# Performance work log

Hardware: AMD Instinct MI355X
Metric: run time of the kernel (lower is better)

Reference implementation:

```python
import jax, jax.numpy as jnp
import numpy as np
from jax import lax

B, T, I, H, C = 64, 512, 512, 1024, 1000


def _lstm_layer(x, W_ih, W_hh, b_ih, b_hh):
    # x: [B, T, in]; W_ih: [4H, in]; W_hh: [4H, H]; biases: [4H]
    # Precompute input projections for all timesteps (one big GEMM).
    xW = jnp.einsum('bti,gi->btg', x, W_ih) + b_ih + b_hh  # [B, T, 4H]
    h0 = jnp.zeros((x.shape[0], W_hh.shape[1]), x.dtype)
    c0 = jnp.zeros_like(h0)

    def step(carry, xw_t):
        h, c = carry
        gates = xw_t + h @ W_hh.T  # [B, 4H]
        i, f, g, o = jnp.split(gates, 4, axis=-1)  # PyTorch gate order i,f,g,o
        i = jax.nn.sigmoid(i)
        f = jax.nn.sigmoid(f)
        g = jnp.tanh(g)
        o = jax.nn.sigmoid(o)
        c = f * c + i * g
        h = o * jnp.tanh(c)
        return (h, c), h

    (h_T, c_T), hs = lax.scan(step, (h0, c0), jnp.swapaxes(xW, 0, 1))
    return jnp.swapaxes(hs, 0, 1), h_T  # [B, T, H], [B, H]


def setup_inputs() -> dict:
    key = jax.random.key(0)
    ks = jax.random.split(key, 11)
    s_i = 1.0 / np.sqrt(H)
    u = lambda k, shape: jax.random.uniform(k, shape, jnp.float32, -s_i, s_i)
    return {
        'x': jax.random.normal(ks[0], (B, T, I), jnp.float32),
        'W_ih0': u(ks[1], (4 * H, I)),
        'W_hh0': u(ks[2], (4 * H, H)),
        'b_ih0': u(ks[3], (4 * H,)),
        'b_hh0': u(ks[4], (4 * H,)),
        'W_ih1': u(ks[5], (4 * H, H)),
        'W_hh1': u(ks[6], (4 * H, H)),
        'b_ih1': u(ks[7], (4 * H,)),
        'b_hh1': u(ks[8], (4 * H,)),
        'W_d': u(ks[9], (C, H)),
        'b_d': u(ks[10], (C,)),
    }


def reference(x, W_ih0, W_hh0, b_ih0, b_hh0, W_ih1, W_hh1, b_ih1, b_hh1, W_d, b_d):
    h1_seq, _ = _lstm_layer(x, W_ih0, W_hh0, b_ih0, b_hh0)
    _, h_last = _lstm_layer(h1_seq, W_ih1, W_hh1, b_ih1, b_hh1)
    return h_last @ W_d.T + b_d  # [B, num_classes]
```

## Files before the change

### kernel.cpp

```cpp
#include <hip/hip_runtime.h>

typedef short short8 __attribute__((ext_vector_type(8)));
typedef float f32x4 __attribute__((ext_vector_type(4)));
typedef float f32x16 __attribute__((ext_vector_type(16)));
typedef int i32x4 __attribute__((ext_vector_type(4)));
typedef unsigned short u16;
typedef unsigned long long u64;

#define NBLK 256
#define BDIM 512
#define BB 64
#define TT 512
#define II 512
#define HH 1024
#define NCLS 1000
#define HBUF (BB*HH)

__device__ __forceinline__ u16 f2bf(float f) {
  union { float f; unsigned u; } v; v.f = f;
  unsigned u = v.u;
  u += 0x7fffu + ((u >> 16) & 1u);
  return (u16)(u >> 16);
}

__device__ __forceinline__ short8 cvt8(f32x4 a, f32x4 b) {
  short8 v;
  v[0] = (short)f2bf(a[0]); v[1] = (short)f2bf(a[1]);
  v[2] = (short)f2bf(a[2]); v[3] = (short)f2bf(a[3]);
  v[4] = (short)f2bf(b[0]); v[5] = (short)f2bf(b[1]);
  v[6] = (short)f2bf(b[2]); v[7] = (short)f2bf(b[3]);
  return v;
}

__device__ __forceinline__ unsigned ld_rlx(const unsigned* p) {
  return __hip_atomic_load(p, __ATOMIC_RELAXED, __HIP_MEMORY_SCOPE_AGENT);
}
__device__ __forceinline__ void st_rlx(unsigned* p, unsigned v) {
  __hip_atomic_store(p, v, __ATOMIC_RELAXED, __HIP_MEMORY_SCOPE_AGENT);
}
__device__ __forceinline__ void wave_wait_ge(const unsigned* p, unsigned tgt) {
  while (ld_rlx(p) < tgt) __builtin_amdgcn_s_sleep(1);
}

__global__ void cvt_x(const float* __restrict__ x, u16* __restrict__ xb, int n8) {
  int i = blockIdx.x * blockDim.x + threadIdx.x;
  const int stride = gridDim.x * blockDim.x;
  for (; i < n8; i += stride) {
    f32x4 a = ((const f32x4*)x)[2 * i];
    f32x4 b = ((const f32x4*)x)[2 * i + 1];
    ((short8*)xb)[i] = cvt8(a, b);
  }
}

#define ISSUE8(arr, OFF)                                                     \
  _Pragma("unroll") for (int i_ = 0; i_ < 8; ++i_)                           \
    asm volatile("global_load_dwordx4 %0, %1, off sc0 sc1"                   \
                 : "=v"(arr[i_]) : "v"(lanep + ((OFF) + i_) * 16));
#define MFMA8(arr, OFF)                                                      \
  _Pragma("unroll") for (int i_ = 0; i_ < 8; ++i_) {                         \
    union { i32x4 q; short8 s; } u_; u_.q = arr[i_];                         \
    acc = __builtin_amdgcn_mfma_f32_32x32x16_bf16(u_.s, breg[B0 + (OFF) + i_],\
                                                  acc, 0, 0, 0); }
#define VMWAIT0 asm volatile("s_waitcnt vmcnt(0)" ::: "memory")
#define VMWAIT8 asm volatile("s_waitcnt vmcnt(8)" ::: "memory")
#define SCHEDB  __builtin_amdgcn_sched_barrier(0)

template<int N, int B0, int MH>
__device__ __forceinline__ void run_coh(const u16* lanep,
                                        const short8 (&breg)[MH], f32x16& acc) {
  static_assert(N == 8 || N == 16 || N == 24 || N == 32, "");
  i32x4 avA[8], avB[8];
  if constexpr (N == 8) {
    ISSUE8(avA, 0);
    VMWAIT0; SCHEDB; MFMA8(avA, 0);
  } else if constexpr (N == 16) {
    ISSUE8(avA, 0); ISSUE8(avB, 8);
    VMWAIT8; SCHEDB; MFMA8(avA, 0);
    VMWAIT0; SCHEDB; MFMA8(avB, 8);
  } else if constexpr (N == 24) {
    ISSUE8(avA, 0); ISSUE8(avB, 8);
    VMWAIT8; SCHEDB; MFMA8(avA, 0); ISSUE8(avA, 16);
    VMWAIT8; SCHEDB; MFMA8(avB, 8);
    VMWAIT0; SCHEDB; MFMA8(avA, 16);
  } else {
    ISSUE8(avA, 0); ISSUE8(avB, 8);
    VMWAIT8; SCHEDB; MFMA8(avA, 0); ISSUE8(avA, 16);
    VMWAIT8; SCHEDB; MFMA8(avB, 8); ISSUE8(avB, 24);
    VMWAIT8; SCHEDB; MFMA8(avA, 16);
    VMWAIT0; SCHEDB; MFMA8(avB, 24);
  }
}

template<int N, int B0, int MH>
__device__ __forceinline__ void run_pb(const u16* lanep,
                                       const short8 (&breg)[MH], f32x16& acc) {
#pragma unroll
  for (int i = 0; i < N; ++i) {
    short8 av = *(const short8*)(lanep + i * 16);
    acc = __builtin_amdgcn_mfma_f32_32x32x16_bf16(av, breg[B0 + i], acc, 0, 0, 0);
  }
}

template<int N, int B0, int MH>
__device__ __forceinline__ void run_pf(const float* lanep,
                                       const short8 (&breg)[MH], f32x16& acc) {
#pragma unroll
  for (int i = 0; i < N; ++i) {
    short8 av = cvt8(*(const f32x4*)(lanep + i * 16),
                     *(const f32x4*)(lanep + i * 16 + 4));
    acc = __builtin_amdgcn_mfma_f32_32x32x16_bf16(av, breg[B0 + i], acc, 0, 0, 0);
  }
}

template<bool XBF>
__global__ __launch_bounds__(BDIM, 2) void lstm2_fused(
    const float* __restrict__ x, const u16* __restrict__ xb,
    const float* __restrict__ Wih0, const float* __restrict__ Whh0,
    const float* __restrict__ bih0, const float* __restrict__ bhh0,
    const float* __restrict__ Wih1, const float* __restrict__ Whh1,
    const float* __restrict__ bih1, const float* __restrict__ bhh1,
    u16* __restrict__ ring,
    u16* __restrict__ h1buf,
    float* __restrict__ h1f,
    unsigned* __restrict__ bar)
{
  __shared__ u16 wlds[32 * 2048];
  __shared__ float blds[32];
  float (*g4)[64][32] = (float(*)[64][32])((char*)wlds + 98304);

  const bool isL1 = (blockIdx.x >= 128);
  const int wgl = isL1 ? (int)blockIdx.x - 128 : (int)blockIdx.x;
  const int j0 = wgl * 8;
  const int KX = isL1 ? HH : II;
  const int RL = KX + HH;
  const int ROWB = RL * 2;
  const float* Wih = isL1 ? Wih1 : Wih0;
  const float* Whh = isL1 ? Whh1 : Whh0;

  {
    const int cpr = RL / 8;
    for (int idx = threadIdx.x; idx < 32 * cpr; idx += BDIM) {
      int n = idx / cpr, cb = idx - n * cpr;
      int r = ((n >> 3) << 10) + j0 + (n & 7);
      int k = cb * 8;
      const float* src = (k < KX) ? (Wih + (size_t)r * KX + k)
                                  : (Whh + (size_t)r * HH + (k - KX));
      f32x4 a = *(const f32x4*)src;
      f32x4 b = *(const f32x4*)(src + 4);
      short8 v = cvt8(a, b);
      unsigned byte = (unsigned)(n * ROWB + k * 2) ^ ((unsigned)(n & 7) << 4);
      *(short8*)((char*)wlds + byte) = v;
    }
    if (threadIdx.x < 32) {
      int n = threadIdx.x;
      int r = ((n >> 3) << 10) + j0 + (n & 7);
      blds[n] = (isL1 ? bih1[r] : bih0[r]) + (isL1 ? bhh1[r] : bhh0[r]);
    }
  }
  __syncthreads();

  const int lane = threadIdx.x & 63;
  const int wid = threadIdx.x >> 6;
  const int mp = wid & 1, kq = wid >> 1;
  const int row_a = mp * 32 + (lane & 31);
  const int sub8 = (lane >> 5) << 3;
  const char* wch = (const char*)wlds;

  const int tb = threadIdx.x >> 3, tj = threadIdx.x & 7;

  unsigned* const arrA = bar;
  unsigned* const relA = bar + 64;
  unsigned* const arrB = bar + 256;
  unsigned* const relB = bar + 320;

  float c_state = 0.f;

  auto step_tail = [&](const f32x16& acc, u16* hout, unsigned ringtgt, bool wf,
                       unsigned* arr, unsigned* rel, int t) {
    const int col = lane & 31;
    const int rbase = mp * 32 + ((lane >> 5) << 2);
#pragma unroll
    for (int r = 0; r < 16; ++r) {
      int brow = rbase + (r & 3) + ((r >> 2) << 3);
      g4[kq][brow][col] = acc[r];
    }
    __syncthreads();
    float gv[4];
#pragma unroll
    for (int g = 0; g < 4; ++g)
      gv[g] = g4[0][tb][g * 8 + tj] + g4[1][tb][g * 8 + tj]
            + g4[2][tb][g * 8 + tj] + g4[3][tb][g * 8 + tj] + blds[g * 8 + tj];
    float gi = 1.f / (1.f + __expf(-gv[0]));
    float gf = 1.f / (1.f + __expf(-gv[1]));
    float e2 = __expf(2.f * fminf(15.f, fmaxf(-15.f, gv[2])));
    float gg = (e2 - 1.f) / (e2 + 1.f);
    float go = 1.f / (1.f + __expf(-gv[3]));
    c_state = gf * c_state + gi * gg;
    float e2c = __expf(2.f * fminf(15.f, fmaxf(-15.f, c_state)));
    float th = (e2c - 1.f) / (e2c + 1.f);
    float hval = go * th;
    if (ringtgt) wave_wait_ge(relB, ringtgt);
    unsigned hu = (unsigned)f2bf(hval);
    unsigned nbv = (unsigned)__shfl_xor((int)hu, 1);
    if ((tj & 1) == 0) {
      unsigned packed = hu | (nbv << 16);
      unsigned* dst = (unsigned*)(hout + (size_t)tb * HH + j0 + tj);
      st_rlx(dst, packed);
    }
    if (wf) h1f[(size_t)tb * HH + j0 + tj] = hval;
    __syncthreads();
    if (threadIdx.x == 0) {
      unsigned old = atomicAdd(arr, 1u);
      if (old == (unsigned)(128 * (t + 1) - 1)) st_rlx(rel, (unsigned)(t + 1));
    }
  };

  if (!isL1) {
    short8 breg[24];
#pragma unroll
    for (int i = 0; i < 24; ++i) {
      int k = (kq * 24 + i) * 16 + sub8;
      unsigned byte = ((unsigned)((lane & 31) * ROWB + k * 2))
                      ^ ((unsigned)(lane & 7) << 4);
      breg[i] = *(const short8*)(wch + byte);
    }
    __syncthreads();

    for (int t = 0; t < TT; ++t) {
      f32x16 acc = {};
      const u16* hb = ring + (size_t)((t + 2) % 3) * HBUF + (size_t)row_a * HH;
      if (XBF) {
        const u16* xl = xb + (size_t)t * II + (size_t)row_a * ((size_t)TT * II)
                        + kq * 384 + sub8;
        if (kq == 0)      run_pb<24, 0>(xl, breg, acc);
        else if (kq == 1) { run_pb<8, 0>(xl, breg, acc);
                            wave_wait_ge(relA, (unsigned)t);
                            run_coh<16, 8>(hb + 0 + sub8, breg, acc); }
        else if (kq == 2) { wave_wait_ge(relA, (unsigned)t);
                            run_coh<24, 0>(hb + 256 + sub8, breg, acc); }
        else              { wave_wait_ge(relA, (unsigned)t);
                            run_coh<24, 0>(hb + 640 + sub8, breg, acc); }
      } else {
        const float* xl = x + (size_t)t * II + (size_t)row_a * ((size_t)TT * II)
                          + kq * 384 + sub8;
        if (kq == 0)      run_pf<24, 0>(xl, breg, acc);
        else if (kq == 1) { run_pf<8, 0>(xl, breg, acc);
                            wave_wait_ge(relA, (unsigned)t);
                            run_coh<16, 8>(hb + 0 + sub8, breg, acc); }
        else if (kq == 2) { wave_wait_ge(relA, (unsigned)t);
                            run_coh<24, 0>(hb + 256 + sub8, breg, acc); }
        else              { wave_wait_ge(relA, (unsigned)t);
                            run_coh<24, 0>(hb + 640 + sub8, breg, acc); }
      }
      step_tail(acc, ring + (size_t)(t % 3) * HBUF,
                (t >= 3) ? (unsigned)(t - 2) : 0u, false, arrA, relA, t);
    }
  } else {
    short8 breg[32];
#pragma unroll
    for (int i = 0; i < 32; ++i) {
      int k = (kq * 32 + i) * 16 + sub8;
      unsigned byte = ((unsigned)((lane & 31) * ROWB + k * 2))
                      ^ ((unsigned)(lane & 7) << 4);
      breg[i] = *(const short8*)(wch + byte);
    }
    __syncthreads();

    for (int t = 0; t < TT; ++t) {
      f32x16 acc = {};
      if (kq < 2) {
        wave_wait_ge(relA, (unsigned)(t + 1));
        const u16* lp = ring + (size_t)(t % 3) * HBUF + (size_t)row_a * HH
                        + kq * 512 + sub8;
        run_coh<32, 0>(lp, breg, acc);
      } else {
        wave_wait_ge(relB, (unsigned)t);
        const u16* lp = h1buf + (size_t)((t + 1) & 1) * HBUF
                        + (size_t)row_a * HH + (kq - 2) * 512 + sub8;
        run_coh<32, 0>(lp, breg, acc);
      }
      step_tail(acc, h1buf + (size_t)(t & 1) * HBUF, 0u, t == TT - 1,
                arrB, relB, t);
    }
  }
}

__global__ void dense_out(const float* __restrict__ h1, const float* __restrict__ Wd,
                          const float* __restrict__ bd, float* __restrict__ out)
{
  const int b  = threadIdx.x & 63;
  const int cl = threadIdx.x >> 6;
  const int cc = blockIdx.x * 4 + cl;
  float acc = 0.f;
  const float* hrow = h1 + (size_t)b * HH;
  const float* wrow = Wd + (size_t)cc * HH;
#pragma unroll 8
  for (int k = 0; k < HH; k += 4) {
    f32x4 hv = *(const f32x4*)(hrow + k);
    f32x4 wv = *(const f32x4*)(wrow + k);
    acc += hv[0] * wv[0] + hv[1] * wv[1] + hv[2] * wv[2] + hv[3] * wv[3];
  }
  out[(size_t)b * NCLS + cc] = acc + bd[cc];
}

extern "C" void kernel_launch(void* const* d_in, const int* in_sizes, int n_in,
                              void* d_out, int out_size, void* d_ws, size_t ws_size,
                              hipStream_t stream)
{
  (void)in_sizes; (void)n_in; (void)out_size;
  const float* x    = (const float*)d_in[0];
  const float* Wih0 = (const float*)d_in[1];
  const float* Whh0 = (const float*)d_in[2];
  const float* bih0 = (const float*)d_in[3];
  const float* bhh0 = (const float*)d_in[4];
  const float* Wih1 = (const float*)d_in[5];
  const float* Whh1 = (const float*)d_in[6];
  const float* bih1 = (const float*)d_in[7];
  const float* bhh1 = (const float*)d_in[8];
  const float* Wd   = (const float*)d_in[9];
  const float* bd   = (const float*)d_in[10];

  unsigned* bar = (unsigned*)d_ws;
  float* h1f  = (float*)((char*)d_ws + 4096);
  u16* h1buf  = (u16*)((char*)d_ws + 272 * 1024);
  u16* ring   = (u16*)((char*)d_ws + 528 * 1024);
  u16* xb     = (u16*)((char*)d_ws + (1u << 20));

  const size_t needA = (1u << 20) + (size_t)BB * TT * II * 2;
  const bool tierA = (ws_size >= needA);

  hipMemsetAsync(d_ws, 0, 912 * 1024, stream);

  if (tierA) {
    hipLaunchKernelGGL(cvt_x, dim3(2048), dim3(256), 0, stream,
                       x, xb, (int)((size_t)BB * TT * II / 8));
    hipLaunchKernelGGL((lstm2_fused<true>), dim3(NBLK), dim3(BDIM), 0, stream,
                       x, xb, Wih0, Whh0, bih0, bhh0, Wih1, Whh1, bih1, bhh1,
                       ring, h1buf, h1f, bar);
  } else {
    hipLaunchKernelGGL((lstm2_fused<false>), dim3(NBLK), dim3(BDIM), 0, stream,
                       x, xb, Wih0, Whh0, bih0, bhh0, Wih1, Whh1, bih1, bhh1,
                       ring, h1buf, h1f, bar);
  }
  hipLaunchKernelGGL(dense_out, dim3(250), dim3(256), 0, stream, h1f, Wd, bd,
                     (float*)d_out);
}
```

Before: 4.866 ms.

## Split grid-wide step barrier into eight group counters polled in parallel

The single global arrival counter per layer, which all 128 blocks hit with one atomicAdd each step, is replaced by eight counters with 16 blocks each, spaced 128 bytes apart. Waiters now poll all eight release flags at once, one per lane, and proceed only when every group has reached the target. The aim is to cut atomic contention and serialization on one cache line in the per-timestep barrier. In exchange, each poll issues eight loads per wave, and the host must zero the larger barrier region.

```diff
diff --git a/kernel.cpp b/kernel.cpp
--- a/kernel.cpp
+++ b/kernel.cpp
@@ -38,8 +38,14 @@
 __device__ __forceinline__ void st_rlx(unsigned* p, unsigned v) {
   __hip_atomic_store(p, v, __ATOMIC_RELAXED, __HIP_MEMORY_SCOPE_AGENT);
 }
-__device__ __forceinline__ void wave_wait_ge(const unsigned* p, unsigned tgt) {
-  while (ld_rlx(p) < tgt) __builtin_amdgcn_s_sleep(1);
+__device__ __forceinline__ void wave_wait_all8(const unsigned* base, unsigned tgt,
+                                               int lane) {
+  const unsigned* p = base + (unsigned)(lane & 7) * 32;
+  for (;;) {
+    unsigned v = ld_rlx(p);
+    if (__all((int)(v >= tgt))) break;
+    __builtin_amdgcn_s_sleep(1);
+  }
 }
 
 __global__ void cvt_x(const float* __restrict__ x, u16* __restrict__ xb, int n8) {
@@ -131,6 +137,7 @@
   const bool isL1 = (blockIdx.x >= 128);
   const int wgl = isL1 ? (int)blockIdx.x - 128 : (int)blockIdx.x;
   const int j0 = wgl * 8;
+  const int grp = wgl >> 4;
   const int KX = isL1 ? HH : II;
   const int RL = KX + HH;
   const int ROWB = RL * 2;
@@ -169,9 +176,9 @@
   const int tb = threadIdx.x >> 3, tj = threadIdx.x & 7;
 
   unsigned* const arrA = bar;
-  unsigned* const relA = bar + 64;
-  unsigned* const arrB = bar + 256;
-  unsigned* const relB = bar + 320;
+  unsigned* const relA = bar + 256;
+  unsigned* const arrB = bar + 512;
+  unsigned* const relB = bar + 768;
 
   float c_state = 0.f;
 
@@ -199,7 +206,7 @@
     float e2c = __expf(2.f * fminf(15.f, fmaxf(-15.f, c_state)));
     float th = (e2c - 1.f) / (e2c + 1.f);
     float hval = go * th;
-    if (ringtgt) wave_wait_ge(relB, ringtgt);
+    if (ringtgt) wave_wait_all8(relB, ringtgt, lane);
     unsigned hu = (unsigned)f2bf(hval);
     unsigned nbv = (unsigned)__shfl_xor((int)hu, 1);
     if ((tj & 1) == 0) {
@@ -210,8 +217,9 @@
     if (wf) h1f[(size_t)tb * HH + j0 + tj] = hval;
     __syncthreads();
     if (threadIdx.x == 0) {
-      unsigned old = atomicAdd(arr, 1u);
-      if (old == (unsigned)(128 * (t + 1) - 1)) st_rlx(rel, (unsigned)(t + 1));
+      unsigned old = atomicAdd(arr + grp * 32, 1u);
+      if (old == (unsigned)(16 * (t + 1) - 1))
+        st_rlx(rel + grp * 32, (unsigned)(t + 1));
     }
   };
 
@@ -234,22 +242,22 @@
                         + kq * 384 + sub8;
         if (kq == 0)      run_pb<24, 0>(xl, breg, acc);
         else if (kq == 1) { run_pb<8, 0>(xl, breg, acc);
-                            wave_wait_ge(relA, (unsigned)t);
+                            wave_wait_all8(relA, (unsigned)t, lane);
                             run_coh<16, 8>(hb + 0 + sub8, breg, acc); }
-        else if (kq == 2) { wave_wait_ge(relA, (unsigned)t);
+        else if (kq == 2) { wave_wait_all8(relA, (unsigned)t, lane);
                             run_coh<24, 0>(hb + 256 + sub8, breg, acc); }
-        else              { wave_wait_ge(relA, (unsigned)t);
+        else              { wave_wait_all8(relA, (unsigned)t, lane);
                             run_coh<24, 0>(hb + 640 + sub8, breg, acc); }
       } else {
         const float* xl = x + (size_t)t * II + (size_t)row_a * ((size_t)TT * II)
                           + kq * 384 + sub8;
         if (kq == 0)      run_pf<24, 0>(xl, breg, acc);
         else if (kq == 1) { run_pf<8, 0>(xl, breg, acc);
-                            wave_wait_ge(relA, (unsigned)t);
+                            wave_wait_all8(relA, (unsigned)t, lane);
                             run_coh<16, 8>(hb + 0 + sub8, breg, acc); }
-        else if (kq == 2) { wave_wait_ge(relA, (unsigned)t);
+        else if (kq == 2) { wave_wait_all8(relA, (unsigned)t, lane);
                             run_coh<24, 0>(hb + 256 + sub8, breg, acc); }
-        else              { wave_wait_ge(relA, (unsigned)t);
+        else              { wave_wait_all8(relA, (unsigned)t, lane);
                             run_coh<24, 0>(hb + 640 + sub8, breg, acc); }
       }
       step_tail(acc, ring + (size_t)(t % 3) * HBUF,
@@ -269,12 +277,12 @@
     for (int t = 0; t < TT; ++t) {
       f32x16 acc = {};
       if (kq < 2) {
-        wave_wait_ge(relA, (unsigned)(t + 1));
+        wave_wait_all8(relA, (unsigned)(t + 1), lane);
         const u16* lp = ring + (size_t)(t % 3) * HBUF + (size_t)row_a * HH
                         + kq * 512 + sub8;
         run_coh<32, 0>(lp, breg, acc);
       } else {
-        wave_wait_ge(relB, (unsigned)t);
+        wave_wait_all8(relB, (unsigned)t, lane);
         const u16* lp = h1buf + (size_t)((t + 1) & 1) * HBUF
                         + (size_t)row_a * HH + (kq - 2) * 512 + sub8;
         run_coh<32, 0>(lp, breg, acc);
```

Measured after the change: 5.280 ms. 8.5% more time.

## Halve persistent blocks with 16 hidden units each and dual accumulators per wave

Applied to the files above, without the earlier changes.

The fused two-layer LSTM kernel now runs 128 persistent blocks (64 per layer) instead of 256, each owning 16 hidden units. Each wave now handles 32 gate rows across all 64 batch rows, using two MFMA accumulators that share the same register-resident weight fragments. Weights are loaded straight from global memory into registers, with the LDS staging copy removed. The aim is to cut the number of blocks taking part in each per-step grid barrier and to reuse each weight register twice. The cost is twice the activation loads and twice the gate math per block on the serial critical path.

```diff
diff --git a/kernel.cpp b/kernel.cpp
--- a/kernel.cpp
+++ b/kernel.cpp
@@ -5,9 +5,8 @@
 typedef float f32x16 __attribute__((ext_vector_type(16)));
 typedef int i32x4 __attribute__((ext_vector_type(4)));
 typedef unsigned short u16;
-typedef unsigned long long u64;
-
-#define NBLK 256
+
+#define NBLK 128
 #define BDIM 512
 #define BB 64
 #define TT 512
@@ -52,63 +51,72 @@
   }
 }
 
-#define ISSUE8(arr, OFF)                                                     \
-  _Pragma("unroll") for (int i_ = 0; i_ < 8; ++i_)                           \
+#define ISSUE42(buf, OFF)                                                    \
+  _Pragma("unroll") for (int i_ = 0; i_ < 4; ++i_) {                         \
     asm volatile("global_load_dwordx4 %0, %1, off sc0 sc1"                   \
-                 : "=v"(arr[i_]) : "v"(lanep + ((OFF) + i_) * 16));
-#define MFMA8(arr, OFF)                                                      \
-  _Pragma("unroll") for (int i_ = 0; i_ < 8; ++i_) {                         \
-    union { i32x4 q; short8 s; } u_; u_.q = arr[i_];                         \
-    acc = __builtin_amdgcn_mfma_f32_32x32x16_bf16(u_.s, breg[B0 + (OFF) + i_],\
-                                                  acc, 0, 0, 0); }
+                 : "=v"(buf[2 * i_])     : "v"(lp0 + ((OFF) + i_) * 16));    \
+    asm volatile("global_load_dwordx4 %0, %1, off sc0 sc1"                   \
+                 : "=v"(buf[2 * i_ + 1]) : "v"(lp1 + ((OFF) + i_) * 16)); }
+#define MFMA42(buf, OFF)                                                     \
+  _Pragma("unroll") for (int i_ = 0; i_ < 4; ++i_) {                         \
+    union { i32x4 q; short8 s; } uA_, uB_;                                   \
+    uA_.q = buf[2 * i_]; uB_.q = buf[2 * i_ + 1];                            \
+    acc0 = __builtin_amdgcn_mfma_f32_32x32x16_bf16(uA_.s,                    \
+             breg[B0 + (OFF) + i_], acc0, 0, 0, 0);                          \
+    acc1 = __builtin_amdgcn_mfma_f32_32x32x16_bf16(uB_.s,                    \
+             breg[B0 + (OFF) + i_], acc1, 0, 0, 0); }
 #define VMWAIT0 asm volatile("s_waitcnt vmcnt(0)" ::: "memory")
 #define VMWAIT8 asm volatile("s_waitcnt vmcnt(8)" ::: "memory")
 #define SCHEDB  __builtin_amdgcn_sched_barrier(0)
 
 template<int N, int B0, int MH>
-__device__ __forceinline__ void run_coh(const u16* lanep,
-                                        const short8 (&breg)[MH], f32x16& acc) {
-  static_assert(N == 8 || N == 16 || N == 24 || N == 32, "");
-  i32x4 avA[8], avB[8];
-  if constexpr (N == 8) {
-    ISSUE8(avA, 0);
-    VMWAIT0; SCHEDB; MFMA8(avA, 0);
-  } else if constexpr (N == 16) {
-    ISSUE8(avA, 0); ISSUE8(avB, 8);
-    VMWAIT8; SCHEDB; MFMA8(avA, 0);
-    VMWAIT0; SCHEDB; MFMA8(avB, 8);
-  } else if constexpr (N == 24) {
-    ISSUE8(avA, 0); ISSUE8(avB, 8);
-    VMWAIT8; SCHEDB; MFMA8(avA, 0); ISSUE8(avA, 16);
-    VMWAIT8; SCHEDB; MFMA8(avB, 8);
-    VMWAIT0; SCHEDB; MFMA8(avA, 16);
-  } else {
-    ISSUE8(avA, 0); ISSUE8(avB, 8);
-    VMWAIT8; SCHEDB; MFMA8(avA, 0); ISSUE8(avA, 16);
-    VMWAIT8; SCHEDB; MFMA8(avB, 8); ISSUE8(avB, 24);
-    VMWAIT8; SCHEDB; MFMA8(avA, 16);
-    VMWAIT0; SCHEDB; MFMA8(avB, 24);
+__device__ __forceinline__ void run_coh2(const u16* lp0, const u16* lp1,
+                                         const short8 (&breg)[MH],
+                                         f32x16& acc0, f32x16& acc1) {
+  static_assert(N % 4 == 0 && N >= 8, "");
+  constexpr int C = N / 4;
+  i32x4 bufA[8], bufB[8];
+  ISSUE42(bufA, 0);
+  ISSUE42(bufB, 4);
+#pragma unroll
+  for (int c = 0; c < C; ++c) {
+    if (c + 2 < C) {
+      VMWAIT8; SCHEDB;
+      if (c & 1) { MFMA42(bufB, c * 4); ISSUE42(bufB, (c + 2) * 4); }
+      else       { MFMA42(bufA, c * 4); ISSUE42(bufA, (c + 2) * 4); }
+    } else if (c + 1 < C) {
+      VMWAIT8; SCHEDB;
+      if (c & 1) { MFMA42(bufB, c * 4); } else { MFMA42(bufA, c * 4); }
+    } else {
+      VMWAIT0; SCHEDB;
+      if (c & 1) { MFMA42(bufB, c * 4); } else { MFMA42(bufA, c * 4); }
+    }
   }
 }
 
 template<int N, int B0, int MH>
-__device__ __forceinline__ void run_pb(const u16* lanep,
-                                       const short8 (&breg)[MH], f32x16& acc) {
+__device__ __forceinline__ void run_px2(const u16* lp0, const u16* lp1,
+                                        const short8 (&breg)[MH],
+                                        f32x16& acc0, f32x16& acc1) {
 #pragma unroll
   for (int i = 0; i < N; ++i) {
-    short8 av = *(const short8*)(lanep + i * 16);
-    acc = __builtin_amdgcn_mfma_f32_32x32x16_bf16(av, breg[B0 + i], acc, 0, 0, 0);
+    short8 a0 = *(const short8*)(lp0 + i * 16);
+    short8 a1 = *(const short8*)(lp1 + i * 16);
+    acc0 = __builtin_amdgcn_mfma_f32_32x32x16_bf16(a0, breg[B0 + i], acc0, 0, 0, 0);
+    acc1 = __builtin_amdgcn_mfma_f32_32x32x16_bf16(a1, breg[B0 + i], acc1, 0, 0, 0);
   }
 }
 
 template<int N, int B0, int MH>
-__device__ __forceinline__ void run_pf(const float* lanep,
-                                       const short8 (&breg)[MH], f32x16& acc) {
+__device__ __forceinline__ void run_pf2(const float* lp0, const float* lp1,
+                                        const short8 (&breg)[MH],
+                                        f32x16& acc0, f32x16& acc1) {
 #pragma unroll
   for (int i = 0; i < N; ++i) {
-    short8 av = cvt8(*(const f32x4*)(lanep + i * 16),
-                     *(const f32x4*)(lanep + i * 16 + 4));
-    acc = __builtin_amdgcn_mfma_f32_32x32x16_bf16(av, breg[B0 + i], acc, 0, 0, 0);
+    short8 a0 = cvt8(*(const f32x4*)(lp0 + i * 16), *(const f32x4*)(lp0 + i * 16 + 4));
+    short8 a1 = cvt8(*(const f32x4*)(lp1 + i * 16), *(const f32x4*)(lp1 + i * 16 + 4));
+    acc0 = __builtin_amdgcn_mfma_f32_32x32x16_bf16(a0, breg[B0 + i], acc0, 0, 0, 0);
+    acc1 = __builtin_amdgcn_mfma_f32_32x32x16_bf16(a1, breg[B0 + i], acc1, 0, 0, 0);
   }
 }
 
@@ -124,94 +132,88 @@
     float* __restrict__ h1f,
     unsigned* __restrict__ bar)
 {
-  __shared__ u16 wlds[32 * 2048];
-  __shared__ float blds[32];
-  float (*g4)[64][32] = (float(*)[64][32])((char*)wlds + 98304);
-
-  const bool isL1 = (blockIdx.x >= 128);
-  const int wgl = isL1 ? (int)blockIdx.x - 128 : (int)blockIdx.x;
-  const int j0 = wgl * 8;
-  const int KX = isL1 ? HH : II;
-  const int RL = KX + HH;
-  const int ROWB = RL * 2;
-  const float* Wih = isL1 ? Wih1 : Wih0;
-  const float* Whh = isL1 ? Whh1 : Whh0;
-
-  {
-    const int cpr = RL / 8;
-    for (int idx = threadIdx.x; idx < 32 * cpr; idx += BDIM) {
-      int n = idx / cpr, cb = idx - n * cpr;
-      int r = ((n >> 3) << 10) + j0 + (n & 7);
-      int k = cb * 8;
-      const float* src = (k < KX) ? (Wih + (size_t)r * KX + k)
-                                  : (Whh + (size_t)r * HH + (k - KX));
-      f32x4 a = *(const f32x4*)src;
-      f32x4 b = *(const f32x4*)(src + 4);
-      short8 v = cvt8(a, b);
-      unsigned byte = (unsigned)(n * ROWB + k * 2) ^ ((unsigned)(n & 7) << 4);
-      *(short8*)((char*)wlds + byte) = v;
-    }
-    if (threadIdx.x < 32) {
-      int n = threadIdx.x;
-      int r = ((n >> 3) << 10) + j0 + (n & 7);
-      blds[n] = (isL1 ? bih1[r] : bih0[r]) + (isL1 ? bhh1[r] : bhh0[r]);
-    }
-  }
-  __syncthreads();
+  __shared__ float g4[4][64][65];
+  __shared__ float blds[64];
+
+  const bool isL1 = (blockIdx.x >= 64);
+  const int wgl = isL1 ? (int)blockIdx.x - 64 : (int)blockIdx.x;
+  const int j0 = wgl * 16;
 
   const int lane = threadIdx.x & 63;
   const int wid = threadIdx.x >> 6;
-  const int mp = wid & 1, kq = wid >> 1;
-  const int row_a = mp * 32 + (lane & 31);
+  const int gr = wid & 1, kq = wid >> 1;
   const int sub8 = (lane >> 5) << 3;
-  const char* wch = (const char*)wlds;
-
-  const int tb = threadIdx.x >> 3, tj = threadIdx.x & 7;
+  const int rl = gr * 32 + (lane & 31);
+  const int rglob = ((rl >> 4) << 10) + j0 + (rl & 15);
+
+  if (threadIdx.x < 64) {
+    int u = threadIdx.x;
+    int r = ((u >> 4) << 10) + j0 + (u & 15);
+    blds[u] = isL1 ? (bih1[r] + bhh1[r]) : (bih0[r] + bhh0[r]);
+  }
+  __syncthreads();
+
+  const int tb = threadIdx.x >> 3;
+  const int uu = (threadIdx.x & 7) << 1;
 
   unsigned* const arrA = bar;
   unsigned* const relA = bar + 64;
-  unsigned* const arrB = bar + 256;
-  unsigned* const relB = bar + 320;
-
-  float c_state = 0.f;
-
-  auto step_tail = [&](const f32x16& acc, u16* hout, unsigned ringtgt, bool wf,
-                       unsigned* arr, unsigned* rel, int t) {
-    const int col = lane & 31;
-    const int rbase = mp * 32 + ((lane >> 5) << 2);
+  unsigned* const arrB = bar + 128;
+  unsigned* const relB = bar + 192;
+
+  float cst0 = 0.f, cst1 = 0.f;
+
+  auto step_tail = [&](const f32x16& acc0, const f32x16& acc1, u16* hout,
+                       unsigned ringtgt, bool wf, unsigned* arr, unsigned* rel,
+                       int t) {
 #pragma unroll
     for (int r = 0; r < 16; ++r) {
-      int brow = rbase + (r & 3) + ((r >> 2) << 3);
-      g4[kq][brow][col] = acc[r];
+      int brow = (r & 3) + ((r >> 2) << 3) + ((lane >> 5) << 2);
+      g4[kq][brow][rl] = acc0[r];
+      g4[kq][brow + 32][rl] = acc1[r];
     }
     __syncthreads();
-    float gv[4];
-#pragma unroll
-    for (int g = 0; g < 4; ++g)
-      gv[g] = g4[0][tb][g * 8 + tj] + g4[1][tb][g * 8 + tj]
-            + g4[2][tb][g * 8 + tj] + g4[3][tb][g * 8 + tj] + blds[g * 8 + tj];
-    float gi = 1.f / (1.f + __expf(-gv[0]));
-    float gf = 1.f / (1.f + __expf(-gv[1]));
-    float e2 = __expf(2.f * fminf(15.f, fmaxf(-15.f, gv[2])));
-    float gg = (e2 - 1.f) / (e2 + 1.f);
-    float go = 1.f / (1.f + __expf(-gv[3]));
-    c_state = gf * c_state + gi * gg;
-    float e2c = __expf(2.f * fminf(15.f, fmaxf(-15.f, c_state)));
-    float th = (e2c - 1.f) / (e2c + 1.f);
-    float hval = go * th;
+    float hva, hvb;
+    {
+      float gi = g4[0][tb][uu] + g4[1][tb][uu] + g4[2][tb][uu] + g4[3][tb][uu] + blds[uu];
+      float gf = g4[0][tb][16+uu] + g4[1][tb][16+uu] + g4[2][tb][16+uu] + g4[3][tb][16+uu] + blds[16+uu];
+      float gg = g4[0][tb][32+uu] + g4[1][tb][32+uu] + g4[2][tb][32+uu] + g4[3][tb][32+uu] + blds[32+uu];
+      float go = g4[0][tb][48+uu] + g4[1][tb][48+uu] + g4[2][tb][48+uu] + g4[3][tb][48+uu] + blds[48+uu];
+      gi = 1.f / (1.f + __expf(-gi));
+      gf = 1.f / (1.f + __expf(-gf));
+      go = 1.f / (1.f + __expf(-go));
+      float e2 = __expf(2.f * fminf(15.f, fmaxf(-15.f, gg)));
+      gg = (e2 - 1.f) / (e2 + 1.f);
+      cst0 = gf * cst0 + gi * gg;
+      float e2c = __expf(2.f * fminf(15.f, fmaxf(-15.f, cst0)));
+      hva = go * (e2c - 1.f) / (e2c + 1.f);
+    }
+    {
+      int u1 = uu + 1;
+      float gi = g4[0][tb][u1] + g4[1][tb][u1] + g4[2][tb][u1] + g4[3][tb][u1] + blds[u1];
+      float gf = g4[0][tb][16+u1] + g4[1][tb][16+u1] + g4[2][tb][16+u1] + g4[3][tb][16+u1] + blds[16+u1];
+      float gg = g4[0][tb][32+u1] + g4[1][tb][32+u1] + g4[2][tb][32+u1] + g4[3][tb][32+u1] + blds[32+u1];
+      float go = g4[0][tb][48+u1] + g4[1][tb][48+u1] + g4[2][tb][48+u1] + g4[3][tb][48+u1] + blds[48+u1];
+      gi = 1.f / (1.f + __expf(-gi));
+      gf = 1.f / (1.f + __expf(-gf));
+      go = 1.f / (1.f + __expf(-go));
+      float e2 = __expf(2.f * fminf(15.f, fmaxf(-15.f, gg)));
+      gg = (e2 - 1.f) / (e2 + 1.f);
+      cst1 = gf * cst1 + gi * gg;
+      float e2c = __expf(2.f * fminf(15.f, fmaxf(-15.f, cst1)));
+      hvb = go * (e2c - 1.f) / (e2c + 1.f);
+    }
     if (ringtgt) wave_wait_ge(relB, ringtgt);
-    unsigned hu = (unsigned)f2bf(hval);
-    unsigned nbv = (unsigned)__shfl_xor((int)hu, 1);
-    if ((tj & 1) == 0) {
-      unsigned packed = hu | (nbv << 16);
-      unsigned* dst = (unsigned*)(hout + (size_t)tb * HH + j0 + tj);
-      st_rlx(dst, packed);
-    }
-    if (wf) h1f[(size_t)tb * HH + j0 + tj] = hval;
+    unsigned packed = (unsigned)f2bf(hva) | ((unsigned)f2bf(hvb) << 16);
+    st_rlx((unsigned*)(hout + (size_t)tb * HH + j0 + uu), packed);
+    if (wf) {
+      h1f[(size_t)tb * HH + j0 + uu] = hva;
+      h1f[(size_t)tb * HH + j0 + uu + 1] = hvb;
+    }
     __syncthreads();
     if (threadIdx.x == 0) {
       unsigned old = atomicAdd(arr, 1u);
-      if (old == (unsigned)(128 * (t + 1) - 1)) st_rlx(rel, (unsigned)(t + 1));
+      if (old == (unsigned)(64 * (t + 1) - 1)) st_rlx(rel, (unsigned)(t + 1));
     }
   };
 
@@ -219,67 +221,71 @@
     short8 breg[24];
 #pragma unroll
     for (int i = 0; i < 24; ++i) {
-      int k = (kq * 24 + i) * 16 + sub8;
-      unsigned byte = ((unsigned)((lane & 31) * ROWB + k * 2))
-                      ^ ((unsigned)(lane & 7) << 4);
-      breg[i] = *(const short8*)(wch + byte);
-    }
-    __syncthreads();
+      int k = kq * 384 + i * 16 + sub8;
+      const float* src = (k < II) ? (Wih0 + (size_t)rglob * II + k)
+                                  : (Whh0 + (size_t)rglob * HH + (k - II));
+      breg[i] = cvt8(*(const f32x4*)src, *(const f32x4*)(src + 4));
+    }
 
     for (int t = 0; t < TT; ++t) {
-      f32x16 acc = {};
-      const u16* hb = ring + (size_t)((t + 2) % 3) * HBUF + (size_t)row_a * HH;
+      f32x16 acc0 = {}, acc1 = {};
+      const u16* hb = ring + (size_t)((t + 2) % 3) * HBUF
+                      + (size_t)(lane & 31) * HH;
+      const u16* hb1 = hb + (size_t)32 * HH;
       if (XBF) {
-        const u16* xl = xb + (size_t)t * II + (size_t)row_a * ((size_t)TT * II)
-                        + kq * 384 + sub8;
-        if (kq == 0)      run_pb<24, 0>(xl, breg, acc);
-        else if (kq == 1) { run_pb<8, 0>(xl, breg, acc);
+        const u16* xl0 = xb + (size_t)(lane & 31) * ((size_t)TT * II)
+                         + (size_t)t * II + kq * 384 + sub8;
+        const u16* xl1 = xl0 + (size_t)32 * TT * II;
+        if (kq == 0)      run_px2<24, 0>(xl0, xl1, breg, acc0, acc1);
+        else if (kq == 1) { run_px2<8, 0>(xl0, xl1, breg, acc0, acc1);
                             wave_wait_ge(relA, (unsigned)t);
-                            run_coh<16, 8>(hb + 0 + sub8, breg, acc); }
+                            run_coh2<16, 8>(hb + sub8, hb1 + sub8, breg, acc0, acc1); }
         else if (kq == 2) { wave_wait_ge(relA, (unsigned)t);
-                            run_coh<24, 0>(hb + 256 + sub8, breg, acc); }
+                            run_coh2<24, 0>(hb + 256 + sub8, hb1 + 256 + sub8, breg, acc0, acc1); }
         else              { wave_wait_ge(relA, (unsigned)t);
-                            run_coh<24, 0>(hb + 640 + sub8, breg, acc); }
+                            run_coh2<24, 0>(hb + 640 + sub8, hb1 + 640 + sub8, breg, acc0, acc1); }
       } else {
-        const float* xl = x + (size_t)t * II + (size_t)row_a * ((size_t)TT * II)
-                          + kq * 384 + sub8;
-        if (kq == 0)      run_pf<24, 0>(xl, breg, acc);
-        else if (kq == 1) { run_pf<8, 0>(xl, breg, acc);
+        const float* xl0 = x + (size_t)(lane & 31) * ((size_t)TT * II)
+                           + (size_t)t * II + kq * 384 + sub8;
+        const float* xl1 = xl0 + (size_t)32 * TT * II;
+        if (kq == 0)      run_pf2<24, 0>(xl0, xl1, breg, acc0, acc1);
+        else if (kq == 1) { run_pf2<8, 0>(xl0, xl1, breg, acc0, acc1);
                             wave_wait_ge(relA, (unsigned)t);
-                            run_coh<16, 8>(hb + 0 + sub8, breg, acc); }
+                            run_coh2<16, 8>(hb + sub8, hb1 + sub8, breg, acc0, acc1); }
         else if (kq == 2) { wave_wait_ge(relA, (unsigned)t);
-                            run_coh<24, 0>(hb + 256 + sub8, breg, acc); }
+                            run_coh2<24, 0>(hb + 256 + sub8, hb1 + 256 + sub8, breg, acc0, acc1); }
         else              { wave_wait_ge(relA, (unsigned)t);
-                            run_coh<24, 0>(hb + 640 + sub8, breg, acc); }
+                            run_coh2<24, 0>(hb + 640 + sub8, hb1 + 640 + sub8, breg, acc0, acc1); }
       }
-      step_tail(acc, ring + (size_t)(t % 3) * HBUF,
+      step_tail(acc0, acc1, ring + (size_t)(t % 3) * HBUF,
                 (t >= 3) ? (unsigned)(t - 2) : 0u, false, arrA, relA, t);
     }
   } else {
     short8 breg[32];
 #pragma unroll
     for (int i = 0; i < 32; ++i) {
-      int k = (kq * 32 + i) * 16 + sub8;
-      unsigned byte = ((unsigned)((lane & 31) * ROWB + k * 2))
-                      ^ ((unsigned)(lane & 7) << 4);
-      breg[i] = *(const short8*)(wch + byte);
-    }
-    __syncthreads();
+      int k = kq * 512 + i * 16 + sub8;
+      const float* src = (k < HH) ? (Wih1 + (size_t)rglob * HH + k)
+                                  : (Whh1 + (size_t)rglob * HH + (k - HH));
+      breg[i] = cvt8(*(const f32x4*)src, *(const f32x4*)(src + 4));
+    }
 
     for (int t = 0; t < TT; ++t) {
-      f32x16 acc = {};
+      f32x16 acc0 = {}, acc1 = {};
       if (kq < 2) {
         wave_wait_ge(relA, (unsigned)(t + 1));
-        const u16* lp = ring + (size_t)(t % 3) * HBUF + (size_t)row_a * HH
-                        + kq * 512 + sub8;
-        run_coh<32, 0>(lp, breg, acc);
+        const u16* lp0 = ring + (size_t)(t % 3) * HBUF
+                         + (size_t)(lane & 31) * HH + kq * 512 + sub8;
+        const u16* lp1 = lp0 + (size_t)32 * HH;
+        run_coh2<32, 0>(lp0, lp1, breg, acc0, acc1);
       } else {
         wave_wait_ge(relB, (unsigned)t);
-        const u16* lp = h1buf + (size_t)((t + 1) & 1) * HBUF
-                        + (size_t)row_a * HH + (kq - 2) * 512 + sub8;
-        run_coh<32, 0>(lp, breg, acc);
+        const u16* lp0 = h1buf + (size_t)((t + 1) & 1) * HBUF
+                         + (size_t)(lane & 31) * HH + (kq - 2) * 512 + sub8;
+        const u16* lp1 = lp0 + (size_t)32 * HH;
+        run_coh2<32, 0>(lp0, lp1, breg, acc0, acc1);
       }
-      step_tail(acc, h1buf + (size_t)(t & 1) * HBUF, 0u, t == TT - 1,
+      step_tail(acc0, acc1, h1buf + (size_t)(t & 1) * HBUF, 0u, t == TT - 1,
                 arrB, relB, t);
     }
   }
```

Measured after the change: 8.367 ms. 1.72x slower.

## Repartition LSTM blocks into 16 units by 32 batch rows, load weights directly

Applied to the files above, without the earlier changes.

Each block now covers 16 hidden units (64 gate rows) for half of the batch (32 rows), where before it covered 8 units (32 gate rows) for all 64 batch rows. The MFMA B operand now spans gate rows and the A operand spans batch rows. Weights are loaded straight from global fp32 into registers and converted to bf16, which removes the large LDS weight staging buffer and its barrier, and the shared memory is shrunk to a padded gate-reduction tile. Each block now reads twice as many weight rows but half as many h and x rows per step; the cost is that weight rows are duplicated across the two batch-half blocks.

```diff
diff --git a/kernel.cpp b/kernel.cpp
--- a/kernel.cpp
+++ b/kernel.cpp
@@ -5,7 +5,6 @@
 typedef float f32x16 __attribute__((ext_vector_type(16)));
 typedef int i32x4 __attribute__((ext_vector_type(4)));
 typedef unsigned short u16;
-typedef unsigned long long u64;
 
 #define NBLK 256
 #define BDIM 512
@@ -124,72 +123,56 @@
     float* __restrict__ h1f,
     unsigned* __restrict__ bar)
 {
-  __shared__ u16 wlds[32 * 2048];
-  __shared__ float blds[32];
-  float (*g4)[64][32] = (float(*)[64][32])((char*)wlds + 98304);
+  __shared__ float g4[4][32][68];
+  __shared__ float blds[64];
 
   const bool isL1 = (blockIdx.x >= 128);
   const int wgl = isL1 ? (int)blockIdx.x - 128 : (int)blockIdx.x;
-  const int j0 = wgl * 8;
-  const int KX = isL1 ? HH : II;
-  const int RL = KX + HH;
-  const int ROWB = RL * 2;
-  const float* Wih = isL1 ? Wih1 : Wih0;
-  const float* Whh = isL1 ? Whh1 : Whh0;
-
-  {
-    const int cpr = RL / 8;
-    for (int idx = threadIdx.x; idx < 32 * cpr; idx += BDIM) {
-      int n = idx / cpr, cb = idx - n * cpr;
-      int r = ((n >> 3) << 10) + j0 + (n & 7);
-      int k = cb * 8;
-      const float* src = (k < KX) ? (Wih + (size_t)r * KX + k)
-                                  : (Whh + (size_t)r * HH + (k - KX));
-      f32x4 a = *(const f32x4*)src;
-      f32x4 b = *(const f32x4*)(src + 4);
-      short8 v = cvt8(a, b);
-      unsigned byte = (unsigned)(n * ROWB + k * 2) ^ ((unsigned)(n & 7) << 4);
-      *(short8*)((char*)wlds + byte) = v;
-    }
-    if (threadIdx.x < 32) {
-      int n = threadIdx.x;
-      int r = ((n >> 3) << 10) + j0 + (n & 7);
-      blds[n] = (isL1 ? bih1[r] : bih0[r]) + (isL1 ? bhh1[r] : bhh0[r]);
-    }
-  }
-  __syncthreads();
+  const int ug = wgl >> 1, bg = wgl & 1;
+  const int j0 = ug * 16;
+  const int rowoff = bg * 32;
 
   const int lane = threadIdx.x & 63;
   const int wid = threadIdx.x >> 6;
-  const int mp = wid & 1, kq = wid >> 1;
-  const int row_a = mp * 32 + (lane & 31);
+  const int gr = wid & 1, kq = wid >> 1;
   const int sub8 = (lane >> 5) << 3;
-  const char* wch = (const char*)wlds;
-
-  const int tb = threadIdx.x >> 3, tj = threadIdx.x & 7;
+  const int rl = gr * 32 + (lane & 31);
+  const int rglob = ((rl >> 4) << 10) + j0 + (rl & 15);
+  const int arow = rowoff + (lane & 31);
+
+  if (threadIdx.x < 64) {
+    int u = threadIdx.x;
+    int r = ((u >> 4) << 10) + j0 + (u & 15);
+    blds[u] = isL1 ? (bih1[r] + bhh1[r]) : (bih0[r] + bhh0[r]);
+  }
+  __syncthreads();
+
+  const int tb = threadIdx.x >> 4;
+  const int tu = threadIdx.x & 15;
 
   unsigned* const arrA = bar;
   unsigned* const relA = bar + 64;
-  unsigned* const arrB = bar + 256;
-  unsigned* const relB = bar + 320;
+  unsigned* const arrB = bar + 128;
+  unsigned* const relB = bar + 192;
 
   float c_state = 0.f;
 
   auto step_tail = [&](const f32x16& acc, u16* hout, unsigned ringtgt, bool wf,
                        unsigned* arr, unsigned* rel, int t) {
     const int col = lane & 31;
-    const int rbase = mp * 32 + ((lane >> 5) << 2);
+    const int rbase = (lane >> 5) << 2;
 #pragma unroll
     for (int r = 0; r < 16; ++r) {
       int brow = rbase + (r & 3) + ((r >> 2) << 3);
-      g4[kq][brow][col] = acc[r];
+      g4[kq][brow][gr * 32 + col] = acc[r];
     }
     __syncthreads();
     float gv[4];
 #pragma unroll
     for (int g = 0; g < 4; ++g)
-      gv[g] = g4[0][tb][g * 8 + tj] + g4[1][tb][g * 8 + tj]
-            + g4[2][tb][g * 8 + tj] + g4[3][tb][g * 8 + tj] + blds[g * 8 + tj];
+      gv[g] = g4[0][tb][g * 16 + tu] + g4[1][tb][g * 16 + tu]
+            + g4[2][tb][g * 16 + tu] + g4[3][tb][g * 16 + tu]
+            + blds[g * 16 + tu];
     float gi = 1.f / (1.f + __expf(-gv[0]));
     float gf = 1.f / (1.f + __expf(-gv[1]));
     float e2 = __expf(2.f * fminf(15.f, fmaxf(-15.f, gv[2])));
@@ -202,12 +185,12 @@
     if (ringtgt) wave_wait_ge(relB, ringtgt);
     unsigned hu = (unsigned)f2bf(hval);
     unsigned nbv = (unsigned)__shfl_xor((int)hu, 1);
-    if ((tj & 1) == 0) {
+    if ((tu & 1) == 0) {
       unsigned packed = hu | (nbv << 16);
-      unsigned* dst = (unsigned*)(hout + (size_t)tb * HH + j0 + tj);
+      unsigned* dst = (unsigned*)(hout + (size_t)(rowoff + tb) * HH + j0 + tu);
       st_rlx(dst, packed);
     }
-    if (wf) h1f[(size_t)tb * HH + j0 + tj] = hval;
+    if (wf) h1f[(size_t)(rowoff + tb) * HH + j0 + tu] = hval;
     __syncthreads();
     if (threadIdx.x == 0) {
       unsigned old = atomicAdd(arr, 1u);
@@ -219,18 +202,17 @@
     short8 breg[24];
 #pragma unroll
     for (int i = 0; i < 24; ++i) {
-      int k = (kq * 24 + i) * 16 + sub8;
-      unsigned byte = ((unsigned)((lane & 31) * ROWB + k * 2))
-                      ^ ((unsigned)(lane & 7) << 4);
-      breg[i] = *(const short8*)(wch + byte);
-    }
-    __syncthreads();
+      int k = kq * 384 + i * 16 + sub8;
+      const float* src = (k < II) ? (Wih0 + (size_t)rglob * II + k)
+                                  : (Whh0 + (size_t)rglob * HH + (k - II));
+      breg[i] = cvt8(*(const f32x4*)src, *(const f32x4*)(src + 4));
+    }
 
     for (int t = 0; t < TT; ++t) {
       f32x16 acc = {};
-      const u16* hb = ring + (size_t)((t + 2) % 3) * HBUF + (size_t)row_a * HH;
+      const u16* hb = ring + (size_t)((t + 2) % 3) * HBUF + (size_t)arow * HH;
       if (XBF) {
-        const u16* xl = xb + (size_t)t * II + (size_t)row_a * ((size_t)TT * II)
+        const u16* xl = xb + (size_t)arow * ((size_t)TT * II) + (size_t)t * II
                         + kq * 384 + sub8;
         if (kq == 0)      run_pb<24, 0>(xl, breg, acc);
         else if (kq == 1) { run_pb<8, 0>(xl, breg, acc);
@@ -241,7 +223,7 @@
         else              { wave_wait_ge(relA, (unsigned)t);
                             run_coh<24, 0>(hb + 640 + sub8, breg, acc); }
       } else {
-        const float* xl = x + (size_t)t * II + (size_t)row_a * ((size_t)TT * II)
+        const float* xl = x + (size_t)arow * ((size_t)TT * II) + (size_t)t * II
                           + kq * 384 + sub8;
         if (kq == 0)      run_pf<24, 0>(xl, breg, acc);
         else if (kq == 1) { run_pf<8, 0>(xl, breg, acc);
@@ -259,24 +241,23 @@
     short8 breg[32];
 #pragma unroll
     for (int i = 0; i < 32; ++i) {
-      int k = (kq * 32 + i) * 16 + sub8;
-      unsigned byte = ((unsigned)((lane & 31) * ROWB + k * 2))
-                      ^ ((unsigned)(lane & 7) << 4);
-      breg[i] = *(const short8*)(wch + byte);
-    }
-    __syncthreads();
+      int k = kq * 512 + i * 16 + sub8;
+      const float* src = (k < HH) ? (Wih1 + (size_t)rglob * HH + k)
+                                  : (Whh1 + (size_t)rglob * HH + (k - HH));
+      breg[i] = cvt8(*(const f32x4*)src, *(const f32x4*)(src + 4));
+    }
 
     for (int t = 0; t < TT; ++t) {
       f32x16 acc = {};
       if (kq < 2) {
         wave_wait_ge(relA, (unsigned)(t + 1));
-        const u16* lp = ring + (size_t)(t % 3) * HBUF + (size_t)row_a * HH
+        const u16* lp = ring + (size_t)(t % 3) * HBUF + (size_t)arow * HH
                         + kq * 512 + sub8;
         run_coh<32, 0>(lp, breg, acc);
       } else {
         wave_wait_ge(relB, (unsigned)t);
         const u16* lp = h1buf + (size_t)((t + 1) & 1) * HBUF
-                        + (size_t)row_a * HH + (kq - 2) * 512 + sub8;
+                        + (size_t)arow * HH + (kq - 2) * 512 + sub8;
         run_coh<32, 0>(lp, breg, acc);
       }
       step_tail(acc, h1buf + (size_t)(t & 1) * HBUF, 0u, t == TT - 1,
```

Measured after the change: 4.669 ms. 1.04x faster.
